# Kernel tuning notes

Measured on AMD Instinct MI355X. Metric: run time of the kernel, lower is better.

Reference implementation:

```python
import jax, jax.numpy as jnp
import numpy as np

N, NA, F = 16384, 256, 2048
GAMMA = 1.5
BN_EPS = 1e-5


def setup_inputs() -> dict:
    key = jax.random.key(0)
    k1, k2, k3, k4, k5 = jax.random.split(key, 5)
    a = jax.random.normal(k1, (N, NA), dtype=jnp.float32)
    ps = jax.random.uniform(k2, (N, F), dtype=jnp.float32)
    lim = 1.0 / np.sqrt(NA)
    W = jax.random.uniform(k3, (F, NA), minval=-lim, maxval=lim, dtype=jnp.float32)
    b = jax.random.uniform(k4, (F,), minval=-lim, maxval=lim, dtype=jnp.float32)
    bn_w = jnp.ones((F,), dtype=jnp.float32)
    bn_b = jnp.zeros((F,), dtype=jnp.float32)
    return {"a": a, "ps": ps, "W": W, "b": b, "bn_w": bn_w, "bn_b": bn_b}


def sparsemax(z):
    # Faithful translation of the repo's Sparsemax (note: it sorts ASCENDING,
    # exactly as the original torch code does).
    D = z.shape[-1]
    s = jnp.sort(z, axis=-1)                      # ascending, [N, D]
    r = jnp.arange(D, dtype=z.dtype)              # [D]
    w = (1.0 + r * s - jnp.cumsum(s, axis=-1) > 0).astype(jnp.int32)
    k_z = jnp.max(jnp.arange(D, dtype=jnp.int32) * w, axis=-1)   # [N]
    m = (jnp.arange(D)[None, :] < (k_z + 1)[:, None]).astype(z.dtype)  # [N, D]
    m_z = jnp.sum(m * s, axis=-1)                 # [N]
    tau_z = (m_z + 1.0) / k_z.astype(z.dtype)     # [N]
    return jnp.maximum(z - tau_z[:, None], 0.0)


def reference(a, ps, W, b, bn_w, bn_b):
    # Linear: (N, n_a) -> (N, F)
    x = a @ W.T + b
    # BatchNorm1d (training mode: batch statistics, biased variance)
    mu = jnp.mean(x, axis=0)
    var = jnp.mean((x - mu) ** 2, axis=0)
    x = (x - mu) / jnp.sqrt(var + BN_EPS) * bn_w + bn_b
    # Sparsemax over prior-scaled activations
    m = sparsemax(x * ps)
    new_ps = ps * (GAMMA - jax.lax.stop_gradient(m))
    return m, new_ps
```

## Files before the change

### kernel.cpp

```cpp
#include <hip/hip_runtime.h>
#include <hip/hip_bf16.h>
#include <math.h>

#define N_ROWS 16384
#define N_A    256
#define N_F    2048
#define GAMMA  1.5f
#define BN_EPS 1e-5f

typedef __attribute__((ext_vector_type(8))) short short8;
typedef __attribute__((ext_vector_type(4))) float f32x4;

__global__ __launch_bounds__(256) void cvt_bf16(const float* __restrict__ in,
                                                unsigned short* __restrict__ out,
                                                int n4) {
    int i = blockIdx.x * 256 + threadIdx.x;
    if (i >= n4) return;
    float4 v = reinterpret_cast<const float4*>(in)[i];
    ushort4 o;
    __hip_bfloat16 hx = __float2bfloat16(v.x);
    __hip_bfloat16 hy = __float2bfloat16(v.y);
    __hip_bfloat16 hz = __float2bfloat16(v.z);
    __hip_bfloat16 hw = __float2bfloat16(v.w);
    o.x = __builtin_bit_cast(unsigned short, hx);
    o.y = __builtin_bit_cast(unsigned short, hy);
    o.z = __builtin_bit_cast(unsigned short, hz);
    o.w = __builtin_bit_cast(unsigned short, hw);
    reinterpret_cast<ushort4*>(out)[i] = o;
}

__global__ __launch_bounds__(256) void gemm_x(const unsigned short* __restrict__ aB,
                                              const unsigned short* __restrict__ wB,
                                              const float* __restrict__ bias,
                                              float* __restrict__ x) {
    const int lane = threadIdx.x & 63;
    const int wave = threadIdx.x >> 6;
    const int r16  = lane & 15;
    const int quad = lane >> 4;
    const int row0 = blockIdx.y * 64 + wave * 16;
    const int col0 = blockIdx.x * 64;

    f32x4 acc[4] = {{0.f,0.f,0.f,0.f},{0.f,0.f,0.f,0.f},
                    {0.f,0.f,0.f,0.f},{0.f,0.f,0.f,0.f}};

    const unsigned short* aRow = aB + (size_t)(row0 + r16) * N_A;
    const unsigned short* wRow0 = wB + (size_t)(col0 + r16) * N_A;

    #pragma unroll
    for (int ks = 0; ks < 8; ++ks) {
        const int k0 = ks * 32 + quad * 8;
        short8 afrag = *reinterpret_cast<const short8*>(aRow + k0);
        #pragma unroll
        for (int t = 0; t < 4; ++t) {
            short8 bfrag = *reinterpret_cast<const short8*>(wRow0 + (size_t)t * 16 * N_A + k0);
            acc[t] = __builtin_amdgcn_mfma_f32_16x16x32_bf16(afrag, bfrag, acc[t], 0, 0, 0);
        }
    }

    #pragma unroll
    for (int t = 0; t < 4; ++t) {
        const int col = col0 + t * 16 + r16;
        const float bcol = bias[col];
        #pragma unroll
        for (int r = 0; r < 4; ++r) {
            const int row = row0 + quad * 4 + r;
            x[(size_t)row * N_F + col] = acc[t][r] + bcol;
        }
    }
}

__global__ __launch_bounds__(256) void colstats_partial(const float* __restrict__ x,
                                                        float* __restrict__ ps1,
                                                        float* __restrict__ ps2) {
    const int f  = blockIdx.x * 256 + threadIdx.x;
    const int rc = blockIdx.y;
    const float* p = x + (size_t)rc * 256 * N_F + f;
    float s1 = 0.f, s2 = 0.f;
    #pragma unroll 4
    for (int n = 0; n < 256; ++n) {
        float v = p[(size_t)n * N_F];
        s1 += v;
        s2 += v * v;
    }
    ps1[rc * N_F + f] = s1;
    ps2[rc * N_F + f] = s2;
}

__global__ __launch_bounds__(256) void finalize_stats(const float* __restrict__ ps1,
                                                      const float* __restrict__ ps2,
                                                      const float* __restrict__ bn_w,
                                                      const float* __restrict__ bn_b,
                                                      float* __restrict__ scale,
                                                      float* __restrict__ shift) {
    const int f = blockIdx.x * 256 + threadIdx.x;
    float s1 = 0.f, s2 = 0.f;
    for (int i = 0; i < 64; ++i) {
        s1 += ps1[i * N_F + f];
        s2 += ps2[i * N_F + f];
    }
    const float inv_n = 1.0f / (float)N_ROWS;
    const float mu  = s1 * inv_n;
    const float var = s2 * inv_n - mu * mu;
    const float sc  = bn_w[f] / sqrtf(var + BN_EPS);
    scale[f] = sc;
    shift[f] = bn_b[f] - mu * sc;
}

__global__ __launch_bounds__(256) void bn_sparsemax(const float* __restrict__ x,
                                                    const float* __restrict__ ps,
                                                    const float* __restrict__ scale,
                                                    const float* __restrict__ shift,
                                                    float* __restrict__ m_out,
                                                    float* __restrict__ ps_out) {
    const int row = blockIdx.x;
    const int tid = threadIdx.x;
    const float* xr = x  + (size_t)row * N_F;
    const float* pr = ps + (size_t)row * N_F;

    float z[8], p[8];
    float s = 0.f, mx = -INFINITY, mn = INFINITY;

    #pragma unroll
    for (int c = 0; c < 2; ++c) {
        const int f = c * 1024 + tid * 4;
        float4 xv = *reinterpret_cast<const float4*>(xr + f);
        float4 pv = *reinterpret_cast<const float4*>(pr + f);
        float4 sc = *reinterpret_cast<const float4*>(scale + f);
        float4 sh = *reinterpret_cast<const float4*>(shift + f);
        float zz;
        zz = (xv.x * sc.x + sh.x) * pv.x; z[c*4+0] = zz; p[c*4+0] = pv.x; s += zz; mx = fmaxf(mx, zz); mn = fminf(mn, zz);
        zz = (xv.y * sc.y + sh.y) * pv.y; z[c*4+1] = zz; p[c*4+1] = pv.y; s += zz; mx = fmaxf(mx, zz); mn = fminf(mn, zz);
        zz = (xv.z * sc.z + sh.z) * pv.z; z[c*4+2] = zz; p[c*4+2] = pv.z; s += zz; mx = fmaxf(mx, zz); mn = fminf(mn, zz);
        zz = (xv.w * sc.w + sh.w) * pv.w; z[c*4+3] = zz; p[c*4+3] = pv.w; s += zz; mx = fmaxf(mx, zz); mn = fminf(mn, zz);
    }

    #pragma unroll
    for (int off = 32; off > 0; off >>= 1) {
        s  += __shfl_xor(s, off);
        mx  = fmaxf(mx, __shfl_xor(mx, off));
        mn  = fminf(mn, __shfl_xor(mn, off));
    }
    __shared__ float rs[4], rmx[4], rmn[4];
    const int wave = tid >> 6;
    if ((tid & 63) == 0) { rs[wave] = s; rmx[wave] = mx; rmn[wave] = mn; }
    __syncthreads();
    s  = rs[0] + rs[1] + rs[2] + rs[3];
    mx = fmaxf(fmaxf(rmx[0], rmx[1]), fmaxf(rmx[2], rmx[3]));
    mn = fminf(fminf(rmn[0], rmn[1]), fminf(rmn[2], rmn[3]));

    const float c_last = 1.0f + (float)(N_F - 1) * mx - s;
    float tau;
    if (c_last > 0.0f) {
        tau = (s + 1.0f) / (float)(N_F - 1);
    } else {
        tau = (mn + 1.0f) / 0.0f;
    }

    float* mo = m_out  + (size_t)row * N_F;
    float* po = ps_out + (size_t)row * N_F;
    #pragma unroll
    for (int c = 0; c < 2; ++c) {
        const int f = c * 1024 + tid * 4;
        float4 mv, pv;
        mv.x = fmaxf(z[c*4+0] - tau, 0.f); pv.x = p[c*4+0] * (GAMMA - mv.x);
        mv.y = fmaxf(z[c*4+1] - tau, 0.f); pv.y = p[c*4+1] * (GAMMA - mv.y);
        mv.z = fmaxf(z[c*4+2] - tau, 0.f); pv.z = p[c*4+2] * (GAMMA - mv.z);
        mv.w = fmaxf(z[c*4+3] - tau, 0.f); pv.w = p[c*4+3] * (GAMMA - mv.w);
        *reinterpret_cast<float4*>(mo + f) = mv;
        *reinterpret_cast<float4*>(po + f) = pv;
    }
}

extern "C" void kernel_launch(void* const* d_in, const int* in_sizes, int n_in,
                              void* d_out, int out_size, void* d_ws, size_t ws_size,
                              hipStream_t stream) {
    const float* a    = (const float*)d_in[0];
    const float* ps   = (const float*)d_in[1];
    const float* W    = (const float*)d_in[2];
    const float* bias = (const float*)d_in[3];
    const float* bnw  = (const float*)d_in[4];
    const float* bnb  = (const float*)d_in[5];

    float* out    = (float*)d_out;
    float* x      = out;
    float* m_out  = out;
    float* ps_out = out + (size_t)N_ROWS * N_F;

    char* ws = (char*)d_ws;
    unsigned short* aB = (unsigned short*)ws;
    unsigned short* wB = (unsigned short*)(ws + 8388608);
    float* ps1   = (float*)(ws + 9437184);
    float* ps2   = (float*)(ws + 9961472);
    float* scale = (float*)(ws + 10485760);
    float* shift = (float*)(ws + 10493952);

    cvt_bf16<<<(N_ROWS * N_A / 4 + 255) / 256, 256, 0, stream>>>(a, aB, N_ROWS * N_A / 4);
    cvt_bf16<<<(N_F * N_A / 4 + 255) / 256, 256, 0, stream>>>(W, wB, N_F * N_A / 4);
    gemm_x<<<dim3(N_F / 64, N_ROWS / 64), 256, 0, stream>>>(aB, wB, bias, x);
    colstats_partial<<<dim3(N_F / 256, 64), 256, 0, stream>>>(x, ps1, ps2);
    finalize_stats<<<N_F / 256, 256, 0, stream>>>(ps1, ps2, bnw, bnb, scale, shift);
    bn_sparsemax<<<N_ROWS, 256, 0, stream>>>(x, ps, scale, shift, m_out, ps_out);
}
```

Before: 558.8 us.

## Fuse column stats into GEMM epilogue and store intermediate x as bf16

The GEMM epilogue now computes per-column sum and sum-of-squares partials via shuffles and shared memory, which removes the separate colstats pass over x. The intermediate x is staged through LDS and written as bf16 into the output buffer, halving its write and read traffic. The GEMM tile grows to 128x128 for more reuse per block. The risk is reduced precision of x before normalization and sparsemax.

```diff
diff --git a/kernel.cpp b/kernel.cpp
--- a/kernel.cpp
+++ b/kernel.cpp
@@ -18,72 +18,94 @@
     if (i >= n4) return;
     float4 v = reinterpret_cast<const float4*>(in)[i];
     ushort4 o;
-    __hip_bfloat16 hx = __float2bfloat16(v.x);
-    __hip_bfloat16 hy = __float2bfloat16(v.y);
-    __hip_bfloat16 hz = __float2bfloat16(v.z);
-    __hip_bfloat16 hw = __float2bfloat16(v.w);
-    o.x = __builtin_bit_cast(unsigned short, hx);
-    o.y = __builtin_bit_cast(unsigned short, hy);
-    o.z = __builtin_bit_cast(unsigned short, hz);
-    o.w = __builtin_bit_cast(unsigned short, hw);
+    o.x = __builtin_bit_cast(unsigned short, __float2bfloat16(v.x));
+    o.y = __builtin_bit_cast(unsigned short, __float2bfloat16(v.y));
+    o.z = __builtin_bit_cast(unsigned short, __float2bfloat16(v.z));
+    o.w = __builtin_bit_cast(unsigned short, __float2bfloat16(v.w));
     reinterpret_cast<ushort4*>(out)[i] = o;
 }
 
 __global__ __launch_bounds__(256) void gemm_x(const unsigned short* __restrict__ aB,
                                               const unsigned short* __restrict__ wB,
                                               const float* __restrict__ bias,
-                                              float* __restrict__ x) {
+                                              unsigned short* __restrict__ xB,
+                                              float* __restrict__ ps1,
+                                              float* __restrict__ ps2) {
     const int lane = threadIdx.x & 63;
     const int wave = threadIdx.x >> 6;
     const int r16  = lane & 15;
     const int quad = lane >> 4;
-    const int row0 = blockIdx.y * 64 + wave * 16;
-    const int col0 = blockIdx.x * 64;
-
-    f32x4 acc[4] = {{0.f,0.f,0.f,0.f},{0.f,0.f,0.f,0.f},
-                    {0.f,0.f,0.f,0.f},{0.f,0.f,0.f,0.f}};
-
-    const unsigned short* aRow = aB + (size_t)(row0 + r16) * N_A;
-    const unsigned short* wRow0 = wB + (size_t)(col0 + r16) * N_A;
+    const int col0 = blockIdx.x * 128;
+    const int rowB = blockIdx.y * 128;
+    const int row0 = rowB + wave * 32;
+
+    f32x4 acc[2][8];
+    #pragma unroll
+    for (int g = 0; g < 2; ++g)
+        #pragma unroll
+        for (int t = 0; t < 8; ++t)
+            acc[g][t] = (f32x4){0.f, 0.f, 0.f, 0.f};
+
+    const unsigned short* aR0 = aB + (size_t)(row0 + r16) * N_A;
+    const unsigned short* aR1 = aR0 + 16 * N_A;
+    const unsigned short* wR  = wB + (size_t)(col0 + r16) * N_A;
 
     #pragma unroll
     for (int ks = 0; ks < 8; ++ks) {
         const int k0 = ks * 32 + quad * 8;
-        short8 afrag = *reinterpret_cast<const short8*>(aRow + k0);
-        #pragma unroll
-        for (int t = 0; t < 4; ++t) {
-            short8 bfrag = *reinterpret_cast<const short8*>(wRow0 + (size_t)t * 16 * N_A + k0);
-            acc[t] = __builtin_amdgcn_mfma_f32_16x16x32_bf16(afrag, bfrag, acc[t], 0, 0, 0);
+        short8 a0 = *reinterpret_cast<const short8*>(aR0 + k0);
+        short8 a1 = *reinterpret_cast<const short8*>(aR1 + k0);
+        #pragma unroll
+        for (int t = 0; t < 8; ++t) {
+            short8 bf = *reinterpret_cast<const short8*>(wR + (size_t)t * 16 * N_A + k0);
+            acc[0][t] = __builtin_amdgcn_mfma_f32_16x16x32_bf16(a0, bf, acc[0][t], 0, 0, 0);
+            acc[1][t] = __builtin_amdgcn_mfma_f32_16x16x32_bf16(a1, bf, acc[1][t], 0, 0, 0);
         }
     }
 
-    #pragma unroll
-    for (int t = 0; t < 4; ++t) {
-        const int col = col0 + t * 16 + r16;
-        const float bcol = bias[col];
-        #pragma unroll
-        for (int r = 0; r < 4; ++r) {
-            const int row = row0 + quad * 4 + r;
-            x[(size_t)row * N_F + col] = acc[t][r] + bcol;
+    __shared__ float cs1[4][128];
+    __shared__ float cs2[4][128];
+    __shared__ unsigned short tile[128][136];
+
+    #pragma unroll
+    for (int t = 0; t < 8; ++t) {
+        const float bcol = bias[col0 + t * 16 + r16];
+        float s1 = 0.f, s2 = 0.f;
+        #pragma unroll
+        for (int g = 0; g < 2; ++g) {
+            #pragma unroll
+            for (int r = 0; r < 4; ++r) {
+                float v = acc[g][t][r] + bcol;
+                s1 += v;
+                s2 += v * v;
+                tile[wave * 32 + g * 16 + quad * 4 + r][t * 16 + r16] =
+                    __builtin_bit_cast(unsigned short, __float2bfloat16(v));
+            }
         }
-    }
-}
-
-__global__ __launch_bounds__(256) void colstats_partial(const float* __restrict__ x,
-                                                        float* __restrict__ ps1,
-                                                        float* __restrict__ ps2) {
-    const int f  = blockIdx.x * 256 + threadIdx.x;
-    const int rc = blockIdx.y;
-    const float* p = x + (size_t)rc * 256 * N_F + f;
-    float s1 = 0.f, s2 = 0.f;
-    #pragma unroll 4
-    for (int n = 0; n < 256; ++n) {
-        float v = p[(size_t)n * N_F];
-        s1 += v;
-        s2 += v * v;
-    }
-    ps1[rc * N_F + f] = s1;
-    ps2[rc * N_F + f] = s2;
+        s1 += __shfl_xor(s1, 16); s1 += __shfl_xor(s1, 32);
+        s2 += __shfl_xor(s2, 16); s2 += __shfl_xor(s2, 32);
+        if (quad == 0) { cs1[wave][t * 16 + r16] = s1; cs2[wave][t * 16 + r16] = s2; }
+    }
+    __syncthreads();
+
+    if (threadIdx.x < 128) {
+        const int c = threadIdx.x;
+        float s1 = cs1[0][c] + cs1[1][c] + cs1[2][c] + cs1[3][c];
+        float s2 = cs2[0][c] + cs2[1][c] + cs2[2][c] + cs2[3][c];
+        ps1[(size_t)blockIdx.y * N_F + col0 + c] = s1;
+        ps2[(size_t)blockIdx.y * N_F + col0 + c] = s2;
+    }
+
+    {
+        const int r = threadIdx.x >> 1;
+        const int h = threadIdx.x & 1;
+        const unsigned short* src = &tile[r][h * 64];
+        unsigned short* dst = xB + (size_t)(rowB + r) * 4096 + col0 + h * 64;
+        #pragma unroll
+        for (int i = 0; i < 8; ++i)
+            *reinterpret_cast<short8*>(dst + i * 8) =
+                *reinterpret_cast<const short8*>(src + i * 8);
+    }
 }
 
 __global__ __launch_bounds__(256) void finalize_stats(const float* __restrict__ ps1,
@@ -94,9 +116,10 @@
                                                       float* __restrict__ shift) {
     const int f = blockIdx.x * 256 + threadIdx.x;
     float s1 = 0.f, s2 = 0.f;
-    for (int i = 0; i < 64; ++i) {
-        s1 += ps1[i * N_F + f];
-        s2 += ps2[i * N_F + f];
+    #pragma unroll 4
+    for (int i = 0; i < 128; ++i) {
+        s1 += ps1[(size_t)i * N_F + f];
+        s2 += ps2[(size_t)i * N_F + f];
     }
     const float inv_n = 1.0f / (float)N_ROWS;
     const float mu  = s1 * inv_n;
@@ -106,32 +129,42 @@
     shift[f] = bn_b[f] - mu * sc;
 }
 
-__global__ __launch_bounds__(256) void bn_sparsemax(const float* __restrict__ x,
+__global__ __launch_bounds__(256) void bn_sparsemax(const unsigned short* xB,
                                                     const float* __restrict__ ps,
                                                     const float* __restrict__ scale,
                                                     const float* __restrict__ shift,
-                                                    float* __restrict__ m_out,
+                                                    float* m_out,
                                                     float* __restrict__ ps_out) {
     const int row = blockIdx.x;
     const int tid = threadIdx.x;
-    const float* xr = x  + (size_t)row * N_F;
-    const float* pr = ps + (size_t)row * N_F;
-
-    float z[8], p[8];
+    const int f0  = tid * 8;
+
+    const unsigned short* xr = xB + (size_t)row * 4096 + f0;
+    const float* pr = ps + (size_t)row * N_F + f0;
+
+    short8 xv = *reinterpret_cast<const short8*>(xr);
+    float4 p0  = *reinterpret_cast<const float4*>(pr);
+    float4 p1  = *reinterpret_cast<const float4*>(pr + 4);
+    float4 sc0 = *reinterpret_cast<const float4*>(scale + f0);
+    float4 sc1 = *reinterpret_cast<const float4*>(scale + f0 + 4);
+    float4 sh0 = *reinterpret_cast<const float4*>(shift + f0);
+    float4 sh1 = *reinterpret_cast<const float4*>(shift + f0 + 4);
+
+    float pv[8]  = {p0.x, p0.y, p0.z, p0.w, p1.x, p1.y, p1.z, p1.w};
+    float scv[8] = {sc0.x, sc0.y, sc0.z, sc0.w, sc1.x, sc1.y, sc1.z, sc1.w};
+    float shv[8] = {sh0.x, sh0.y, sh0.z, sh0.w, sh1.x, sh1.y, sh1.z, sh1.w};
+
+    float z[8];
     float s = 0.f, mx = -INFINITY, mn = INFINITY;
-
-    #pragma unroll
-    for (int c = 0; c < 2; ++c) {
-        const int f = c * 1024 + tid * 4;
-        float4 xv = *reinterpret_cast<const float4*>(xr + f);
-        float4 pv = *reinterpret_cast<const float4*>(pr + f);
-        float4 sc = *reinterpret_cast<const float4*>(scale + f);
-        float4 sh = *reinterpret_cast<const float4*>(shift + f);
-        float zz;
-        zz = (xv.x * sc.x + sh.x) * pv.x; z[c*4+0] = zz; p[c*4+0] = pv.x; s += zz; mx = fmaxf(mx, zz); mn = fminf(mn, zz);
-        zz = (xv.y * sc.y + sh.y) * pv.y; z[c*4+1] = zz; p[c*4+1] = pv.y; s += zz; mx = fmaxf(mx, zz); mn = fminf(mn, zz);
-        zz = (xv.z * sc.z + sh.z) * pv.z; z[c*4+2] = zz; p[c*4+2] = pv.z; s += zz; mx = fmaxf(mx, zz); mn = fminf(mn, zz);
-        zz = (xv.w * sc.w + sh.w) * pv.w; z[c*4+3] = zz; p[c*4+3] = pv.w; s += zz; mx = fmaxf(mx, zz); mn = fminf(mn, zz);
+    #pragma unroll
+    for (int i = 0; i < 8; ++i) {
+        float xf = __builtin_bit_cast(float,
+                       (unsigned int)((unsigned short)xv[i]) << 16);
+        float zz = (xf * scv[i] + shv[i]) * pv[i];
+        z[i] = zz;
+        s += zz;
+        mx = fmaxf(mx, zz);
+        mn = fminf(mn, zz);
     }
 
     #pragma unroll
@@ -156,19 +189,21 @@
         tau = (mn + 1.0f) / 0.0f;
     }
 
-    float* mo = m_out  + (size_t)row * N_F;
-    float* po = ps_out + (size_t)row * N_F;
-    #pragma unroll
-    for (int c = 0; c < 2; ++c) {
-        const int f = c * 1024 + tid * 4;
-        float4 mv, pv;
-        mv.x = fmaxf(z[c*4+0] - tau, 0.f); pv.x = p[c*4+0] * (GAMMA - mv.x);
-        mv.y = fmaxf(z[c*4+1] - tau, 0.f); pv.y = p[c*4+1] * (GAMMA - mv.y);
-        mv.z = fmaxf(z[c*4+2] - tau, 0.f); pv.z = p[c*4+2] * (GAMMA - mv.z);
-        mv.w = fmaxf(z[c*4+3] - tau, 0.f); pv.w = p[c*4+3] * (GAMMA - mv.w);
-        *reinterpret_cast<float4*>(mo + f) = mv;
-        *reinterpret_cast<float4*>(po + f) = pv;
-    }
+    float* mo = m_out  + (size_t)row * N_F + f0;
+    float* po = ps_out + (size_t)row * N_F + f0;
+    float4 mv0, mv1, po0, po1;
+    mv0.x = fmaxf(z[0] - tau, 0.f); po0.x = pv[0] * (GAMMA - mv0.x);
+    mv0.y = fmaxf(z[1] - tau, 0.f); po0.y = pv[1] * (GAMMA - mv0.y);
+    mv0.z = fmaxf(z[2] - tau, 0.f); po0.z = pv[2] * (GAMMA - mv0.z);
+    mv0.w = fmaxf(z[3] - tau, 0.f); po0.w = pv[3] * (GAMMA - mv0.w);
+    mv1.x = fmaxf(z[4] - tau, 0.f); po1.x = pv[4] * (GAMMA - mv1.x);
+    mv1.y = fmaxf(z[5] - tau, 0.f); po1.y = pv[5] * (GAMMA - mv1.y);
+    mv1.z = fmaxf(z[6] - tau, 0.f); po1.z = pv[6] * (GAMMA - mv1.z);
+    mv1.w = fmaxf(z[7] - tau, 0.f); po1.w = pv[7] * (GAMMA - mv1.w);
+    *reinterpret_cast<float4*>(mo)     = mv0;
+    *reinterpret_cast<float4*>(mo + 4) = mv1;
+    *reinterpret_cast<float4*>(po)     = po0;
+    *reinterpret_cast<float4*>(po + 4) = po1;
 }
 
 extern "C" void kernel_launch(void* const* d_in, const int* in_sizes, int n_in,
@@ -182,22 +217,21 @@
     const float* bnb  = (const float*)d_in[5];
 
     float* out    = (float*)d_out;
-    float* x      = out;
     float* m_out  = out;
     float* ps_out = out + (size_t)N_ROWS * N_F;
+    unsigned short* xB = (unsigned short*)d_out;
 
     char* ws = (char*)d_ws;
     unsigned short* aB = (unsigned short*)ws;
-    unsigned short* wB = (unsigned short*)(ws + 8388608);
-    float* ps1   = (float*)(ws + 9437184);
-    float* ps2   = (float*)(ws + 9961472);
-    float* scale = (float*)(ws + 10485760);
-    float* shift = (float*)(ws + 10493952);
-
-    cvt_bf16<<<(N_ROWS * N_A / 4 + 255) / 256, 256, 0, stream>>>(a, aB, N_ROWS * N_A / 4);
-    cvt_bf16<<<(N_F * N_A / 4 + 255) / 256, 256, 0, stream>>>(W, wB, N_F * N_A / 4);
-    gemm_x<<<dim3(N_F / 64, N_ROWS / 64), 256, 0, stream>>>(aB, wB, bias, x);
-    colstats_partial<<<dim3(N_F / 256, 64), 256, 0, stream>>>(x, ps1, ps2);
+    unsigned short* wB = (unsigned short*)(ws + (8u << 20));
+    float* ps1   = (float*)(ws + (9u  << 20));
+    float* ps2   = (float*)(ws + (10u << 20));
+    float* scale = (float*)(ws + (11u << 20));
+    float* shift = (float*)(ws + (11u << 20) + 8192);
+
+    cvt_bf16<<<4096, 256, 0, stream>>>(a, aB, N_ROWS * N_A / 4);
+    cvt_bf16<<<512, 256, 0, stream>>>(W, wB, N_F * N_A / 4);
+    gemm_x<<<dim3(N_F / 128, N_ROWS / 128), 256, 0, stream>>>(aB, wB, bias, xB, ps1, ps2);
     finalize_stats<<<N_F / 256, 256, 0, stream>>>(ps1, ps2, bnw, bnb, scale, shift);
-    bn_sparsemax<<<N_ROWS, 256, 0, stream>>>(x, ps, scale, shift, m_out, ps_out);
-}
+    bn_sparsemax<<<N_ROWS, 256, 0, stream>>>(xB, ps, scale, shift, m_out, ps_out);
+}
```

Result: faster. 492.3 us (-11.9%).
